# Kernel tuning notes

Hardware: AMD Instinct MI355X
Metric: run time of the kernel (lower is better)

Reference implementation:

```python
import jax, jax.numpy as jnp
import numpy as np

N_S = 50000
N_T = 50000
E = 800000
D_IN = 128
D_OUT = 128


def setup_inputs() -> dict:
    key = jax.random.key(0)
    k1, k2, k3, k4 = jax.random.split(key, 4)
    edge_index = jax.random.randint(k1, (2, E), 0, N_S, dtype=jnp.int64)
    x_s = jax.random.normal(k2, (N_S, D_IN), dtype=jnp.float32)
    x_t = jax.random.normal(k3, (N_T, D_IN), dtype=jnp.float32)
    # glorot-ish linear weight of GCNConv (bias=False)
    W = jax.random.normal(k4, (D_IN, D_OUT), dtype=jnp.float32) * (1.0 / np.sqrt(D_IN))
    return {"edge_index": edge_index, "x_s": x_s, "x_t": x_t, "W": W}


def reference(edge_index, x_s, x_t, W):
    N_s = x_s.shape[0]
    N_t = x_t.shape[0]
    N = N_s + N_t
    # dropout p=0.0 -> identity; concat bipartite features
    x = jnp.concatenate([x_s, x_t], axis=0)  # [N, d_in]
    row = edge_index[0]
    col = edge_index[1] + N_s  # module shifts target indices in-place
    # GCNConv: add self-loops with weight 1
    loops = jnp.arange(N, dtype=row.dtype)
    row_f = jnp.concatenate([row, loops])
    col_f = jnp.concatenate([col, loops])
    w = jnp.ones(row_f.shape[0], dtype=x.dtype)
    # symmetric degree normalization: deg computed on target (col)
    deg = jax.ops.segment_sum(w, col_f, num_segments=N)
    deg_inv_sqrt = jnp.where(deg > 0, jax.lax.rsqrt(deg), 0.0)
    norm = deg_inv_sqrt[row_f] * deg_inv_sqrt[col_f]  # [E+N]
    # linear transform then normalized scatter-add aggregation
    h = x @ W  # [N, d_out]
    msg = h[row_f] * norm[:, None]  # gather + scale, [E+N, d_out]
    out = jax.ops.segment_sum(msg, col_f, num_segments=N)  # scatter-add
    out = jax.nn.relu(out)
    return out[:N_s], out[N_s:]
```

## Files before the change

### kernel.cpp

```cpp
#include <hip/hip_runtime.h>
#include <hip/hip_bf16.h>
#include <math.h>

#define NSRC 50000
#define NTGT 50000
#define NTOT 100000
#define NEDGE 800000
#define DIM 128

#define NBUCK 1563
#define BCAP 768
#define BPAD 16
#define BLK 512
#define EPT 4
#define EPB 2048
#define PBLK 391
#define GEMM_GRID 782

typedef __attribute__((ext_vector_type(8))) short short8;
typedef __attribute__((ext_vector_type(4))) float float4v;

union U8 { short8 s; uint4 u; };

__device__ __forceinline__ unsigned short f2bf(float f) {
    unsigned u = __float_as_uint(f);
    unsigned r = (u + 0x7FFFu + ((u >> 16) & 1u)) >> 16;
    return (unsigned short)r;
}
__device__ __forceinline__ float bf2f(unsigned us) {
    return __uint_as_float(us << 16);
}
__device__ __forceinline__ unsigned pkbf(float lo, float hi) {
    __hip_bfloat162 b = __float22bfloat162_rn(make_float2(lo, hi));
    return *(unsigned*)&b;
}

__global__ __launch_bounds__(256) void k_prep(const float* __restrict__ W,
                                              unsigned short* __restrict__ Wt,
                                              int* __restrict__ bcnt) {
    int i = blockIdx.x * 256 + threadIdx.x;
    if (i < NBUCK * BPAD) bcnt[i] = 0;
    if (i < DIM * DIM) {
        int j = i & 7, lane = (i >> 3) & 63, ts = i >> 9;
        int t = ts >> 2, s = ts & 3;
        int nl = lane & 15, qd = lane >> 4;
        Wt[i] = f2bf(W[(s * 32 + qd * 8 + j) * DIM + (t * 16 + nl)]);
    }
}

__global__ __launch_bounds__(BLK) void k_part(const int* __restrict__ row,
                                              const int* __restrict__ col,
                                              int* __restrict__ bcnt,
                                              unsigned* __restrict__ part) {
    __shared__ int hist[NBUCK], runbase[NBUCK], cur[NBUCK];
    int tid = threadIdx.x;
    for (int i = tid; i < NBUCK; i += BLK) hist[i] = 0;
    __syncthreads();

    int e0 = blockIdx.x * EPB + tid * EPT;
    bool valid = (e0 + EPT <= NEDGE);
    int c[EPT], r[EPT];
    if (valid) {
        *(int4*)&c[0] = *(const int4*)(col + e0);
        *(int4*)&r[0] = *(const int4*)(row + e0);
#pragma unroll
        for (int i = 0; i < EPT; ++i) atomicAdd(&hist[c[i] >> 5], 1);
    }
    __syncthreads();
    for (int i = tid; i < NBUCK; i += BLK) {
        runbase[i] = atomicAdd(&bcnt[i * BPAD], hist[i]);
        cur[i] = 0;
    }
    __syncthreads();
    if (valid) {
#pragma unroll
        for (int i = 0; i < EPT; ++i) {
            int q = c[i] >> 5;
            int pos = runbase[q] + atomicAdd(&cur[q], 1);
            part[q * BCAP + pos] = (unsigned)r[i] | ((unsigned)(c[i] & 31) << 16);
        }
    }
}

__global__ __launch_bounds__(BLK) void k_gemm(const float* __restrict__ xsrc,
                                              const float* __restrict__ xtgt,
                                              const unsigned short* __restrict__ Wt,
                                              unsigned short* __restrict__ h,
                                              float* __restrict__ out) {
    __shared__ unsigned short Bs[DIM * DIM];

    const int tid = threadIdx.x;
    for (int idx = tid; idx < 2048; idx += BLK)
        ((uint4*)Bs)[idx] = ((const uint4*)Wt)[idx];

    const int wave = tid >> 6, lane = tid & 63;
    const int nl = lane & 15, quad = lane >> 4;

    int node = blockIdx.x * 128 + wave * 16 + nl;
    int mc = (node < NTOT) ? node : (NTOT - 1);
    const float* xrow = (mc < NSRC) ? (xsrc + (size_t)mc * DIM)
                                    : (xtgt + (size_t)(mc - NSRC) * DIM);
    float4 a[8];
#pragma unroll
    for (int s = 0; s < 4; ++s) {
        a[2 * s]     = *(const float4*)(xrow + s * 32 + quad * 8);
        a[2 * s + 1] = *(const float4*)(xrow + s * 32 + quad * 8 + 4);
    }
    __syncthreads();

    float4v acc[8];
#pragma unroll
    for (int t = 0; t < 8; ++t) acc[t] = (float4v){0.f, 0.f, 0.f, 0.f};

#pragma unroll
    for (int s = 0; s < 4; ++s) {
        U8 af;
        af.u.x = pkbf(a[2 * s].x, a[2 * s].y);
        af.u.y = pkbf(a[2 * s].z, a[2 * s].w);
        af.u.z = pkbf(a[2 * s + 1].x, a[2 * s + 1].y);
        af.u.w = pkbf(a[2 * s + 1].z, a[2 * s + 1].w);
#pragma unroll
        for (int t = 0; t < 8; ++t) {
            short8 bf = *(const short8*)&Bs[((t * 4 + s) * 64 + lane) * 8];
            acc[t] = __builtin_amdgcn_mfma_f32_16x16x32_bf16(bf, af.s, acc[t], 0, 0, 0);
        }
    }

    if (node < NTOT) {
        unsigned short* hp = h + (size_t)node * DIM + quad * 4;
        float* op = out + (size_t)node * DIM + quad * 4;
        bool isrc = (node < NSRC);
#pragma unroll
        for (int t = 0; t < 8; ++t) {
            uint2 p;
            p.x = pkbf(acc[t][0], acc[t][1]);
            p.y = pkbf(acc[t][2], acc[t][3]);
            *(uint2*)(hp + t * 16) = p;
            if (isrc) {
                float4 o;
                o.x = fmaxf(acc[t][0], 0.f);
                o.y = fmaxf(acc[t][1], 0.f);
                o.z = fmaxf(acc[t][2], 0.f);
                o.w = fmaxf(acc[t][3], 0.f);
                *(float4*)(op + t * 16) = o;
            }
        }
    }
}

__global__ __launch_bounds__(BLK) void k_back(const int* __restrict__ bcnt,
                                              const unsigned* __restrict__ part,
                                              const unsigned short* __restrict__ h,
                                              float* __restrict__ out) {
    __shared__ unsigned ebuf[BCAP];
    __shared__ unsigned short srt[BCAP];
    __shared__ int hist[32], st[32], cur[32], bufA[32], bufB[32];

    int q = blockIdx.x, tid = threadIdx.x;
    int n = bcnt[q * BPAD];
    int base = q * BCAP;

    if (tid < 32) hist[tid] = 0;
    __syncthreads();
    for (int i = tid; i < n; i += BLK) {
        unsigned p = part[base + i];
        ebuf[i] = p;
        atomicAdd(&hist[p >> 16], 1);
    }
    __syncthreads();

    if (tid < 32) bufA[tid] = hist[tid];
    int* src = bufA; int* dst = bufB;
    for (int d = 1; d < 32; d <<= 1) {
        __syncthreads();
        if (tid < 32) dst[tid] = src[tid] + ((tid >= d) ? src[tid - d] : 0);
        int* tp = src; src = dst; dst = tp;
    }
    __syncthreads();
    if (tid < 32) { int e = src[tid] - hist[tid]; st[tid] = e; cur[tid] = e; }
    __syncthreads();
    for (int i = tid; i < n; i += BLK) {
        unsigned p = ebuf[i];
        int pos = atomicAdd(&cur[p >> 16], 1);
        srt[pos] = (unsigned short)(p & 0xffffu);
    }
    __syncthreads();

    int w = tid >> 6, lane = tid & 63;
    int qd = lane >> 4, ql = lane & 15;
    int cl0 = w * 4;

    for (int pr = 0; pr < 2; ++pr) {
        int ca = cl0 + pr * 2, cb = ca + 1;
        int nA = hist[ca], sA = st[ca];
        int nB = hist[cb], sB = st[cb];

        float accA[8], accB[8];
#pragma unroll
        for (int i = 0; i < 8; ++i) { accA[i] = 0.f; accB[i] = 0.f; }

        int itA = (nA + 3) >> 2, itB = (nB + 3) >> 2;
        int itn = (itA > itB) ? itA : itB;
        for (int k = 0; k < itn; ++k) {
            int e = 4 * k + qd;
            if (e < nA) {
                int r = (int)srt[sA + e];
                uint4 d = *(const uint4*)(h + (size_t)r * DIM + ql * 8);
                accA[0] += bf2f(d.x & 0xffff); accA[1] += bf2f(d.x >> 16);
                accA[2] += bf2f(d.y & 0xffff); accA[3] += bf2f(d.y >> 16);
                accA[4] += bf2f(d.z & 0xffff); accA[5] += bf2f(d.z >> 16);
                accA[6] += bf2f(d.w & 0xffff); accA[7] += bf2f(d.w >> 16);
            }
            if (e < nB) {
                int r = (int)srt[sB + e];
                uint4 d = *(const uint4*)(h + (size_t)r * DIM + ql * 8);
                accB[0] += bf2f(d.x & 0xffff); accB[1] += bf2f(d.x >> 16);
                accB[2] += bf2f(d.y & 0xffff); accB[3] += bf2f(d.y >> 16);
                accB[4] += bf2f(d.z & 0xffff); accB[5] += bf2f(d.z >> 16);
                accB[6] += bf2f(d.w & 0xffff); accB[7] += bf2f(d.w >> 16);
            }
        }

#pragma unroll
        for (int i = 0; i < 8; ++i) {
            accA[i] += __shfl_xor(accA[i], 16, 64);
            accA[i] += __shfl_xor(accA[i], 32, 64);
            accB[i] += __shfl_xor(accB[i], 16, 64);
            accB[i] += __shfl_xor(accB[i], 32, 64);
        }

        int c0 = q * 32 + ca;
        if (qd == 0 && c0 < NTGT) {
            float di = rsqrtf(1.0f + (float)nA);
            float dd = di * di;
            uint4 dh = *(const uint4*)(h + (size_t)(NSRC + c0) * DIM + ql * 8);
            float4 o0, o1;
            o0.x = fmaxf(di * accA[0] + dd * bf2f(dh.x & 0xffff), 0.f);
            o0.y = fmaxf(di * accA[1] + dd * bf2f(dh.x >> 16), 0.f);
            o0.z = fmaxf(di * accA[2] + dd * bf2f(dh.y & 0xffff), 0.f);
            o0.w = fmaxf(di * accA[3] + dd * bf2f(dh.y >> 16), 0.f);
            o1.x = fmaxf(di * accA[4] + dd * bf2f(dh.z & 0xffff), 0.f);
            o1.y = fmaxf(di * accA[5] + dd * bf2f(dh.z >> 16), 0.f);
            o1.z = fmaxf(di * accA[6] + dd * bf2f(dh.w & 0xffff), 0.f);
            o1.w = fmaxf(di * accA[7] + dd * bf2f(dh.w >> 16), 0.f);
            float* op = out + (size_t)(NSRC + c0) * DIM + ql * 8;
            *(float4*)op = o0;
            *(float4*)(op + 4) = o1;
        }
        int c1 = q * 32 + cb;
        if (qd == 0 && c1 < NTGT) {
            float di = rsqrtf(1.0f + (float)nB);
            float dd = di * di;
            uint4 dh = *(const uint4*)(h + (size_t)(NSRC + c1) * DIM + ql * 8);
            float4 o0, o1;
            o0.x = fmaxf(di * accB[0] + dd * bf2f(dh.x & 0xffff), 0.f);
            o0.y = fmaxf(di * accB[1] + dd * bf2f(dh.x >> 16), 0.f);
            o0.z = fmaxf(di * accB[2] + dd * bf2f(dh.y & 0xffff), 0.f);
            o0.w = fmaxf(di * accB[3] + dd * bf2f(dh.y >> 16), 0.f);
            o1.x = fmaxf(di * accB[4] + dd * bf2f(dh.z & 0xffff), 0.f);
            o1.y = fmaxf(di * accB[5] + dd * bf2f(dh.z >> 16), 0.f);
            o1.z = fmaxf(di * accB[6] + dd * bf2f(dh.w & 0xffff), 0.f);
            o1.w = fmaxf(di * accB[7] + dd * bf2f(dh.w >> 16), 0.f);
            float* op = out + (size_t)(NSRC + c1) * DIM + ql * 8;
            *(float4*)op = o0;
            *(float4*)(op + 4) = o1;
        }
    }
}

extern "C" void kernel_launch(void* const* d_in, const int* in_sizes, int n_in,
                              void* d_out, int out_size, void* d_ws, size_t ws_size,
                              hipStream_t stream) {
    const int* ei     = (const int*)d_in[0];
    const float* xsrc = (const float*)d_in[1];
    const float* xtgt = (const float*)d_in[2];
    const float* W    = (const float*)d_in[3];
    float* out = (float*)d_out;

    const int* row = ei;
    const int* col = ei + NEDGE;

    char* ws = (char*)d_ws;
    unsigned short* h  = (unsigned short*)ws;  ws += (size_t)NTOT * DIM * 2;
    unsigned short* Wt = (unsigned short*)ws;  ws += DIM * DIM * 2;
    unsigned* part = (unsigned*)ws;            ws += (size_t)NBUCK * BCAP * 4;
    int* bcnt = (int*)ws;                      ws += NBUCK * BPAD * 4;

    k_prep<<<98, 256, 0, stream>>>(W, Wt, bcnt);
    k_part<<<PBLK, BLK, 0, stream>>>(row, col, bcnt, part);
    k_gemm<<<GEMM_GRID, BLK, 0, stream>>>(xsrc, xtgt, Wt, h, out);
    k_back<<<NBUCK, BLK, 0, stream>>>(bcnt, part, h, out);
}
```

Measured before the change: 185.7 us.

## Fuse edge partition and GEMM into one launch; widen buckets to 64 targets

```diff
diff --git a/kernel.cpp b/kernel.cpp
--- a/kernel.cpp
+++ b/kernel.cpp
@@ -8,14 +8,15 @@
 #define NEDGE 800000
 #define DIM 128
 
-#define NBUCK 1563
-#define BCAP 768
+#define NBUCK 782
+#define BCAP 1536
 #define BPAD 16
 #define BLK 512
 #define EPT 4
-#define EPB 2048
-#define PBLK 391
+#define EPB2 2048
+#define PBLK2 391
 #define GEMM_GRID 782
+#define FGRID 1173
 
 typedef __attribute__((ext_vector_type(8))) short short8;
 typedef __attribute__((ext_vector_type(4))) float float4v;
@@ -40,63 +41,68 @@
                                               int* __restrict__ bcnt) {
     int i = blockIdx.x * 256 + threadIdx.x;
     if (i < NBUCK * BPAD) bcnt[i] = 0;
-    if (i < DIM * DIM) {
-        int j = i & 7, lane = (i >> 3) & 63, ts = i >> 9;
-        int t = ts >> 2, s = ts & 3;
-        int nl = lane & 15, qd = lane >> 4;
-        Wt[i] = f2bf(W[(s * 32 + qd * 8 + j) * DIM + (t * 16 + nl)]);
-    }
-}
-
-__global__ __launch_bounds__(BLK) void k_part(const int* __restrict__ row,
-                                              const int* __restrict__ col,
-                                              int* __restrict__ bcnt,
-                                              unsigned* __restrict__ part) {
-    __shared__ int hist[NBUCK], runbase[NBUCK], cur[NBUCK];
-    int tid = threadIdx.x;
-    for (int i = tid; i < NBUCK; i += BLK) hist[i] = 0;
-    __syncthreads();
-
-    int e0 = blockIdx.x * EPB + tid * EPT;
-    bool valid = (e0 + EPT <= NEDGE);
-    int c[EPT], r[EPT];
-    if (valid) {
-        *(int4*)&c[0] = *(const int4*)(col + e0);
-        *(int4*)&r[0] = *(const int4*)(row + e0);
-#pragma unroll
-        for (int i = 0; i < EPT; ++i) atomicAdd(&hist[c[i] >> 5], 1);
-    }
-    __syncthreads();
-    for (int i = tid; i < NBUCK; i += BLK) {
-        runbase[i] = atomicAdd(&bcnt[i * BPAD], hist[i]);
-        cur[i] = 0;
-    }
-    __syncthreads();
-    if (valid) {
-#pragma unroll
-        for (int i = 0; i < EPT; ++i) {
-            int q = c[i] >> 5;
-            int pos = runbase[q] + atomicAdd(&cur[q], 1);
-            part[q * BCAP + pos] = (unsigned)r[i] | ((unsigned)(c[i] & 31) << 16);
-        }
-    }
-}
-
-__global__ __launch_bounds__(BLK) void k_gemm(const float* __restrict__ xsrc,
-                                              const float* __restrict__ xtgt,
-                                              const unsigned short* __restrict__ Wt,
-                                              unsigned short* __restrict__ h,
-                                              float* __restrict__ out) {
-    __shared__ unsigned short Bs[DIM * DIM];
+    int j = i & 7, lane = (i >> 3) & 63, ts = i >> 9;
+    int t = ts >> 2, s = ts & 3;
+    int nl = lane & 15, qd = lane >> 4;
+    Wt[i] = f2bf(W[(s * 32 + qd * 8 + j) * DIM + (t * 16 + nl)]);
+}
+
+__global__ __launch_bounds__(BLK) void k_front(const int* __restrict__ row,
+                                               const int* __restrict__ col,
+                                               int* __restrict__ bcnt,
+                                               unsigned* __restrict__ part,
+                                               const float* __restrict__ xsrc,
+                                               const float* __restrict__ xtgt,
+                                               const unsigned short* __restrict__ Wt,
+                                               unsigned short* __restrict__ h,
+                                               float* __restrict__ out) {
+    __shared__ union SM {
+        struct { int hist[NBUCK]; int runbase[NBUCK]; int cur[NBUCK]; } p;
+        unsigned short Bs[DIM * DIM];
+    } sm;
 
     const int tid = threadIdx.x;
+    const int bid = blockIdx.x;
+
+    if (bid % 3 == 0) {
+        for (int i = tid; i < NBUCK; i += BLK) sm.p.hist[i] = 0;
+        __syncthreads();
+
+        int e0 = (bid / 3) * EPB2 + tid * EPT;
+        bool valid = (e0 + EPT <= NEDGE);
+        int c[EPT], r[EPT];
+        if (valid) {
+            *(int4*)&c[0] = *(const int4*)(col + e0);
+            *(int4*)&r[0] = *(const int4*)(row + e0);
+#pragma unroll
+            for (int i = 0; i < EPT; ++i) atomicAdd(&sm.p.hist[c[i] >> 6], 1);
+        }
+        __syncthreads();
+        for (int i = tid; i < NBUCK; i += BLK) {
+            sm.p.runbase[i] = atomicAdd(&bcnt[i * BPAD], sm.p.hist[i]);
+            sm.p.cur[i] = 0;
+        }
+        __syncthreads();
+        if (valid) {
+#pragma unroll
+            for (int i = 0; i < EPT; ++i) {
+                int q = c[i] >> 6;
+                int pos = sm.p.runbase[q] + atomicAdd(&sm.p.cur[q], 1);
+                part[q * BCAP + pos] = (unsigned)r[i] | ((unsigned)(c[i] & 63) << 16);
+            }
+        }
+        return;
+    }
+
+    const int gb = bid - bid / 3 - 1;
+
     for (int idx = tid; idx < 2048; idx += BLK)
-        ((uint4*)Bs)[idx] = ((const uint4*)Wt)[idx];
+        ((uint4*)sm.Bs)[idx] = ((const uint4*)Wt)[idx];
 
     const int wave = tid >> 6, lane = tid & 63;
     const int nl = lane & 15, quad = lane >> 4;
 
-    int node = blockIdx.x * 128 + wave * 16 + nl;
+    int node = gb * 128 + wave * 16 + nl;
     int mc = (node < NTOT) ? node : (NTOT - 1);
     const float* xrow = (mc < NSRC) ? (xsrc + (size_t)mc * DIM)
                                     : (xtgt + (size_t)(mc - NSRC) * DIM);
@@ -121,7 +127,7 @@
         af.u.w = pkbf(a[2 * s + 1].z, a[2 * s + 1].w);
 #pragma unroll
         for (int t = 0; t < 8; ++t) {
-            short8 bf = *(const short8*)&Bs[((t * 4 + s) * 64 + lane) * 8];
+            short8 bf = *(const short8*)&sm.Bs[((t * 4 + s) * 64 + lane) * 8];
             acc[t] = __builtin_amdgcn_mfma_f32_16x16x32_bf16(bf, af.s, acc[t], 0, 0, 0);
         }
     }
@@ -154,13 +160,13 @@
                                               float* __restrict__ out) {
     __shared__ unsigned ebuf[BCAP];
     __shared__ unsigned short srt[BCAP];
-    __shared__ int hist[32], st[32], cur[32], bufA[32], bufB[32];
+    __shared__ int hist[64], bufA[64], bufB[64], cur[64], st[64];
 
     int q = blockIdx.x, tid = threadIdx.x;
     int n = bcnt[q * BPAD];
     int base = q * BCAP;
 
-    if (tid < 32) hist[tid] = 0;
+    if (tid < 64) hist[tid] = 0;
     __syncthreads();
     for (int i = tid; i < n; i += BLK) {
         unsigned p = part[base + i];
@@ -169,15 +175,19 @@
     }
     __syncthreads();
 
-    if (tid < 32) bufA[tid] = hist[tid];
+    if (tid < 64) bufA[tid] = hist[tid];
     int* src = bufA; int* dst = bufB;
-    for (int d = 1; d < 32; d <<= 1) {
+    for (int d = 1; d < 64; d <<= 1) {
         __syncthreads();
-        if (tid < 32) dst[tid] = src[tid] + ((tid >= d) ? src[tid - d] : 0);
+        if (tid < 64) dst[tid] = src[tid] + ((tid >= d) ? src[tid - d] : 0);
         int* tp = src; src = dst; dst = tp;
     }
     __syncthreads();
-    if (tid < 32) { int e = src[tid] - hist[tid]; st[tid] = e; cur[tid] = e; }
+    if (tid < 64) {
+        int excl = src[tid] - hist[tid];
+        cur[tid] = excl;
+        st[tid] = excl;
+    }
     __syncthreads();
     for (int i = tid; i < n; i += BLK) {
         unsigned p = ebuf[i];
@@ -188,9 +198,9 @@
 
     int w = tid >> 6, lane = tid & 63;
     int qd = lane >> 4, ql = lane & 15;
-    int cl0 = w * 4;
-
-    for (int pr = 0; pr < 2; ++pr) {
+    int cl0 = w * 8;
+
+    for (int pr = 0; pr < 4; ++pr) {
         int ca = cl0 + pr * 2, cb = ca + 1;
         int nA = hist[ca], sA = st[ca];
         int nB = hist[cb], sB = st[cb];
@@ -229,7 +239,7 @@
             accB[i] += __shfl_xor(accB[i], 32, 64);
         }
 
-        int c0 = q * 32 + ca;
+        int c0 = q * 64 + ca;
         if (qd == 0 && c0 < NTGT) {
             float di = rsqrtf(1.0f + (float)nA);
             float dd = di * di;
@@ -247,7 +257,7 @@
             *(float4*)op = o0;
             *(float4*)(op + 4) = o1;
         }
-        int c1 = q * 32 + cb;
+        int c1 = q * 64 + cb;
         if (qd == 0 && c1 < NTGT) {
             float di = rsqrtf(1.0f + (float)nB);
             float dd = di * di;
@@ -286,8 +296,7 @@
     unsigned* part = (unsigned*)ws;            ws += (size_t)NBUCK * BCAP * 4;
     int* bcnt = (int*)ws;                      ws += NBUCK * BPAD * 4;
 
-    k_prep<<<98, 256, 0, stream>>>(W, Wt, bcnt);
-    k_part<<<PBLK, BLK, 0, stream>>>(row, col, bcnt, part);
-    k_gemm<<<GEMM_GRID, BLK, 0, stream>>>(xsrc, xtgt, Wt, h, out);
+    k_prep<<<64, 256, 0, stream>>>(W, Wt, bcnt);
+    k_front<<<FGRID, BLK, 0, stream>>>(row, col, bcnt, part, xsrc, xtgt, Wt, h, out);
     k_back<<<NBUCK, BLK, 0, stream>>>(bcnt, part, h, out);
 }
```

Measured after the change: 164.6 us. 11.3% less time.
